# Kernel tuning notes

Measured on AMD Instinct MI355X. Metric: run time of the kernel, lower is better.

The kernel has to match this reference:

```python
import jax, jax.numpy as jnp
import numpy as np

# Config (matches init_kwargs)
B, L, D = 2, 2048, 1024
QH, KVH, HD, FFN = 8, 2, 128, 4096
EPS = 1.1920929e-07  # torch RMSNorm default eps = finfo(float32).eps


def _rope_ts():
    d2 = HD // 2
    freq_exp = (2.0 / HD) * jnp.arange(d2, dtype=jnp.float32)
    return 10000.0 ** freq_exp  # [d2]


def _rope(x):
    # x: [B, L, H, HD], rotated in fp32 (matches x.float() in source)
    d2 = HD // 2
    pos = jnp.arange(L, dtype=jnp.float32)
    rad = pos[:, None] / _rope_ts()[None, :]          # [L, d2]
    s = jnp.sin(rad)[None, :, None, :]                # [1, L, 1, d2]
    c = jnp.cos(rad)[None, :, None, :]
    xf = x.astype(jnp.float32)
    x1, x2 = xf[..., :d2], xf[..., d2:]
    return jnp.concatenate([x1 * c - x2 * s, x2 * c + x1 * s], axis=-1).astype(x.dtype)


def _rmsnorm(x, w):
    xf = x.astype(jnp.float32)
    r = jax.lax.rsqrt(jnp.mean(xf * xf, axis=-1, keepdims=True) + EPS)
    return (xf * r).astype(x.dtype) * w


def setup_inputs() -> dict:
    key = jax.random.key(0)
    ks = jax.random.split(key, 9)
    s = 0.02
    return {
        "x": jax.random.normal(ks[0], (B, L, D), dtype=jnp.float32),
        "ln1_w": jnp.ones((D,), dtype=jnp.float32),
        "wq": jax.random.normal(ks[1], (D, QH * HD), dtype=jnp.float32) * s,
        "wk": jax.random.normal(ks[2], (D, KVH * HD), dtype=jnp.float32) * s,
        "wv": jax.random.normal(ks[3], (D, KVH * HD), dtype=jnp.float32) * s,
        "wo": jax.random.normal(ks[4], (QH * HD, D), dtype=jnp.float32) * s,
        "ln2_w": jnp.ones((D,), dtype=jnp.float32),
        "wg": jax.random.normal(ks[5], (D, FFN), dtype=jnp.float32) * s,
        "wu": jax.random.normal(ks[6], (D, FFN), dtype=jnp.float32) * s,
        "wd": jax.random.normal(ks[7], (FFN, D), dtype=jnp.float32) * s,
    }


def reference(x, ln1_w, wq, wk, wv, wo, ln2_w, wg, wu, wd):
    residual = x
    h = _rmsnorm(x, ln1_w)

    q = _rope((h @ wq).reshape(B, L, QH, HD))          # [B,L,QH,HD]
    k = _rope((h @ wk).reshape(B, L, KVH, HD))         # [B,L,KVH,HD]
    v = (h @ wv).reshape(B, L, KVH, HD)

    rep = QH // KVH  # kv_map = floor(arange(QH)*KVH/QH) == repeat each kv head `rep` times
    qh = jnp.transpose(q, (0, 2, 1, 3)).astype(jnp.float32)                       # [B,QH,L,HD]
    kh = jnp.transpose(jnp.repeat(k, rep, axis=2), (0, 2, 1, 3)).astype(jnp.float32)
    vh = jnp.transpose(jnp.repeat(v, rep, axis=2), (0, 2, 1, 3)).astype(jnp.float32)

    scores = jnp.einsum("bhqd,bhkd->bhqk", qh, kh) / jnp.sqrt(jnp.float32(HD))    # [B,QH,L,L]
    causal = jnp.triu(jnp.ones((L, L), dtype=bool), 1)
    scores = jnp.where(causal, -jnp.inf, scores)
    attn = jax.nn.softmax(scores, axis=-1)
    ctx = jnp.einsum("bhqk,bhkd->bhqd", attn, vh)                                 # [B,QH,L,HD]
    ctx = jnp.transpose(ctx, (0, 2, 1, 3)).reshape(B, L, QH * HD).astype(x.dtype)

    x = ctx @ wo + residual
    residual = x
    h = _rmsnorm(x, ln2_w)
    return (jax.nn.silu(h @ wg) * (h @ wu)) @ wd + residual
```

## Files before the change

kernel.cpp:

```cpp
#include <hip/hip_runtime.h>
#include <hip/hip_bf16.h>
#include <math.h>

#define B_ 2
#define L_ 2048
#define D_ 1024
#define QH_ 8
#define KVH_ 2
#define HD_ 128
#define FFN_ 4096
#define T_ (B_ * L_)
#define EPS_ 1.1920929e-07f

typedef __bf16 bf16x8 __attribute__((ext_vector_type(8)));
typedef float floatx4 __attribute__((ext_vector_type(4)));
typedef unsigned short ushortx8 __attribute__((ext_vector_type(8)));
typedef unsigned short ushortx4 __attribute__((ext_vector_type(4)));

__device__ __forceinline__ unsigned short f2bf(float f) {
  union { float f; unsigned int u; } v;
  v.f = f;
  unsigned int r = v.u + 0x7FFFu + ((v.u >> 16) & 1u);
  return (unsigned short)(r >> 16);
}
__device__ __forceinline__ float bf2f(unsigned short u) {
  union { unsigned int u; float f; } v;
  v.u = ((unsigned int)u) << 16;
  return v.f;
}
__device__ __forceinline__ void gload_lds16(const void* g, void* l) {
  __builtin_amdgcn_global_load_lds((const __attribute__((address_space(1))) void*)g,
                                   (__attribute__((address_space(3))) void*)l, 16, 0, 0);
}

__device__ __forceinline__ void tile_tc(const float* __restrict__ in,
                                        unsigned short* __restrict__ out,
                                        int K, int N, int n0, int k0) {
  __shared__ float tile[32][33];
  int t = threadIdx.x;
  int tx = t & 31, ty = t >> 5;
  for (int r = ty; r < 32; r += 8) tile[r][tx] = in[(size_t)(k0 + r) * N + n0 + tx];
  __syncthreads();
  int nr = t >> 3, kq = t & 7;
  ushortx4 o4;
#pragma unroll
  for (int j = 0; j < 4; j++) o4[j] = f2bf(tile[kq * 4 + j][nr]);
  *(ushortx4*)(out + (size_t)(n0 + nr) * K + k0 + kq * 4) = o4;
}

__device__ __forceinline__ void rmsnorm_row(const float* __restrict__ x,
                                            const float* __restrict__ w,
                                            unsigned short* __restrict__ o, int row) {
  __shared__ float red[4];
  int t = threadIdx.x;
  const float* xr = x + (size_t)row * D_;
  float4 xv = *(const float4*)(xr + t * 4);
  float ss = xv.x * xv.x + xv.y * xv.y + xv.z * xv.z + xv.w * xv.w;
#pragma unroll
  for (int off = 32; off >= 1; off >>= 1) ss += __shfl_xor(ss, off);
  if ((t & 63) == 0) red[t >> 6] = ss;
  __syncthreads();
  float total = red[0] + red[1] + red[2] + red[3];
  float r = rsqrtf(total * (1.0f / (float)D_) + EPS_);
  float4 wv = *(const float4*)(w + t * 4);
  unsigned short* op = o + (size_t)row * D_ + t * 4;
  op[0] = f2bf(xv.x * r * wv.x);
  op[1] = f2bf(xv.y * r * wv.y);
  op[2] = f2bf(xv.z * r * wv.z);
  op[3] = f2bf(xv.w * r * wv.w);
}

__global__ __launch_bounds__(256) void prep_all(
    const float* __restrict__ wq, const float* __restrict__ wk,
    const float* __restrict__ wv, const float* __restrict__ wo,
    const float* __restrict__ wg, const float* __restrict__ wu,
    const float* __restrict__ wd, unsigned short* __restrict__ wT,
    const float* __restrict__ x, const float* __restrict__ ln1w,
    unsigned short* __restrict__ h_bf) {
  int bid = blockIdx.x;
  if (bid < 14848) {
    const float* in;
    unsigned short* out;
    int K, N, nt, base;
    if (bid < 1024)       { in = wq; out = wT;            K = 1024; N = 1024; nt = 32;  base = 0; }
    else if (bid < 1280)  { in = wk; out = wT + 1048576;  K = 1024; N = 256;  nt = 8;   base = 1024; }
    else if (bid < 1536)  { in = wv; out = wT + 1310720;  K = 1024; N = 256;  nt = 8;   base = 1280; }
    else if (bid < 2560)  { in = wo; out = wT + 1572864;  K = 1024; N = 1024; nt = 32;  base = 1536; }
    else if (bid < 6656)  { in = wg; out = wT + 2621440;  K = 1024; N = 4096; nt = 128; base = 2560; }
    else if (bid < 10752) { in = wu; out = wT + 6815744;  K = 1024; N = 4096; nt = 128; base = 6656; }
    else                  { in = wd; out = wT + 11010048; K = 4096; N = 1024; nt = 32;  base = 10752; }
    int idx = bid - base;
    tile_tc(in, out, K, N, (idx % nt) * 32, (idx / nt) * 32);
  } else {
    rmsnorm_row(x, ln1w, h_bf, bid - 14848);
  }
}

__global__ __launch_bounds__(256) void rmsnorm_bf16_kernel(const float* __restrict__ x,
                                                           const float* __restrict__ w,
                                                           unsigned short* __restrict__ o) {
  rmsnorm_row(x, w, o, blockIdx.x);
}

template <int EPI, int MW>
__global__ __launch_bounds__(256) void gemm_bf16(const unsigned short* __restrict__ A,
                                                 const unsigned short* __restrict__ BT,
                                                 const float* __restrict__ R,
                                                 float* __restrict__ C,
                                                 unsigned short* __restrict__ Cb,
                                                 int M, int N, int K) {
  constexpr int AI = MW / 16;
  __shared__ unsigned short As[2][2 * MW * 32];
  __shared__ unsigned short Bs[2][128 * 32];
  int t = threadIdx.x;
  int lane = t & 63, wave = t >> 6;
  int m0 = blockIdx.y * (2 * MW), n0 = blockIdx.x * 128;

  int row_a = t >> 2;
  int kc = ((t & 3) ^ ((t >> 3) & 3)) * 8;
  const unsigned short* ga0 = A + (size_t)(m0 + row_a) * K + kc;
  const unsigned short* ga1 = A + (size_t)(m0 + 64 + row_a) * K + kc;
  const unsigned short* gb0 = BT + (size_t)(n0 + row_a) * K + kc;
  const unsigned short* gb1 = BT + (size_t)(n0 + 64 + row_a) * K + kc;

  int wm = (wave & 1) * MW, wn = (wave >> 1) * 64;
  int fr = lane & 15, quad = lane >> 4;
  int sw = (quad ^ ((fr >> 1) & 3)) * 8;

  floatx4 acc[AI][4];
#pragma unroll
  for (int i = 0; i < AI; i++)
#pragma unroll
    for (int j = 0; j < 4; j++) acc[i][j] = (floatx4){0.f, 0.f, 0.f, 0.f};

  for (int k0 = 0; k0 < K; k0 += 64) {
#pragma unroll
    for (int h = 0; h < 2; h++) {
      int ko = k0 + h * 32;
      gload_lds16(ga0 + ko, As[h] + wave * 512);
      if (MW == 64) gload_lds16(ga1 + ko, As[h] + 2048 + wave * 512);
      gload_lds16(gb0 + ko, Bs[h] + wave * 512);
      gload_lds16(gb1 + ko, Bs[h] + 2048 + wave * 512);
    }
    __syncthreads();
#pragma unroll
    for (int h = 0; h < 2; h++) {
      const unsigned short* arp = As[h] + (size_t)(wm + fr) * 32 + sw;
      const unsigned short* brp = Bs[h] + (size_t)(wn + fr) * 32 + sw;
      bf16x8 af[AI], bfr[4];
#pragma unroll
      for (int i = 0; i < AI; i++)
        af[i] = __builtin_bit_cast(bf16x8, *(const ushortx8*)(arp + i * 16 * 32));
#pragma unroll
      for (int j = 0; j < 4; j++)
        bfr[j] = __builtin_bit_cast(bf16x8, *(const ushortx8*)(brp + j * 16 * 32));
#pragma unroll
      for (int i = 0; i < AI; i++)
#pragma unroll
        for (int j = 0; j < 4; j++)
          acc[i][j] = __builtin_amdgcn_mfma_f32_16x16x32_bf16(af[i], bfr[j], acc[i][j], 0, 0, 0);
    }
    __syncthreads();
  }

  int orow = m0 + wm + quad * 4;
  int ocol = n0 + wn + fr;
#pragma unroll
  for (int i = 0; i < AI; i++) {
#pragma unroll
    for (int r = 0; r < 4; r++) {
      int row = orow + i * 16 + r;
#pragma unroll
      for (int j = 0; j < 4; j++) {
        size_t idx = (size_t)row * N + ocol + j * 16;
        float v = acc[i][j][r];
        if (EPI == 0) C[idx] = v;
        else if (EPI == 1) C[idx] = v + R[idx];
        else if (EPI == 2) C[idx] = v + C[idx];
        else Cb[idx] = f2bf(v);
      }
    }
  }
}

__global__ __launch_bounds__(256, 2) void gemm_gateup(const unsigned short* __restrict__ A,
                                                      const unsigned short* __restrict__ BgT,
                                                      const unsigned short* __restrict__ BuT,
                                                      unsigned short* __restrict__ Cb,
                                                      int M, int K) {
  constexpr int N = FFN_;
  __shared__ unsigned short As[2][128 * 32];
  __shared__ unsigned short Bgs[2][128 * 32];
  __shared__ unsigned short Bus[2][128 * 32];
  int t = threadIdx.x;
  int lane = t & 63, wave = t >> 6;
  int m0 = blockIdx.y * 128, n0 = blockIdx.x * 128;

  int row_a = t >> 2;
  int kc = ((t & 3) ^ ((t >> 3) & 3)) * 8;
  const unsigned short* ga0 = A + (size_t)(m0 + row_a) * K + kc;
  const unsigned short* ga1 = A + (size_t)(m0 + 64 + row_a) * K + kc;
  const unsigned short* gg0 = BgT + (size_t)(n0 + row_a) * K + kc;
  const unsigned short* gg1 = BgT + (size_t)(n0 + 64 + row_a) * K + kc;
  const unsigned short* gu0 = BuT + (size_t)(n0 + row_a) * K + kc;
  const unsigned short* gu1 = BuT + (size_t)(n0 + 64 + row_a) * K + kc;

  int wm = (wave & 1) * 64, wn = (wave >> 1) * 64;
  int fr = lane & 15, quad = lane >> 4;
  int sw = (quad ^ ((fr >> 1) & 3)) * 8;

  floatx4 accg[4][4], accu[4][4];
#pragma unroll
  for (int i = 0; i < 4; i++)
#pragma unroll
    for (int j = 0; j < 4; j++) {
      accg[i][j] = (floatx4){0.f, 0.f, 0.f, 0.f};
      accu[i][j] = (floatx4){0.f, 0.f, 0.f, 0.f};
    }

  for (int k0 = 0; k0 < K; k0 += 64) {
#pragma unroll
    for (int h = 0; h < 2; h++) {
      int ko = k0 + h * 32;
      gload_lds16(ga0 + ko, As[h] + wave * 512);
      gload_lds16(ga1 + ko, As[h] + 2048 + wave * 512);
      gload_lds16(gg0 + ko, Bgs[h] + wave * 512);
      gload_lds16(gg1 + ko, Bgs[h] + 2048 + wave * 512);
      gload_lds16(gu0 + ko, Bus[h] + wave * 512);
      gload_lds16(gu1 + ko, Bus[h] + 2048 + wave * 512);
    }
    __syncthreads();
#pragma unroll
    for (int h = 0; h < 2; h++) {
      const unsigned short* arp = As[h] + (size_t)(wm + fr) * 32 + sw;
      const unsigned short* grp = Bgs[h] + (size_t)(wn + fr) * 32 + sw;
      const unsigned short* urp = Bus[h] + (size_t)(wn + fr) * 32 + sw;
      bf16x8 af[4], bg[4], bu[4];
#pragma unroll
      for (int i = 0; i < 4; i++) {
        af[i] = __builtin_bit_cast(bf16x8, *(const ushortx8*)(arp + i * 16 * 32));
        bg[i] = __builtin_bit_cast(bf16x8, *(const ushortx8*)(grp + i * 16 * 32));
        bu[i] = __builtin_bit_cast(bf16x8, *(const ushortx8*)(urp + i * 16 * 32));
      }
#pragma unroll
      for (int i = 0; i < 4; i++)
#pragma unroll
        for (int j = 0; j < 4; j++) {
          accg[i][j] = __builtin_amdgcn_mfma_f32_16x16x32_bf16(af[i], bg[j], accg[i][j], 0, 0, 0);
          accu[i][j] = __builtin_amdgcn_mfma_f32_16x16x32_bf16(af[i], bu[j], accu[i][j], 0, 0, 0);
        }
    }
    __syncthreads();
  }

  int orow = m0 + wm + quad * 4;
  int ocol = n0 + wn + fr;
#pragma unroll
  for (int i = 0; i < 4; i++) {
#pragma unroll
    for (int r = 0; r < 4; r++) {
      int row = orow + i * 16 + r;
#pragma unroll
      for (int j = 0; j < 4; j++) {
        float g = accg[i][j][r];
        float u = accu[i][j][r];
        Cb[(size_t)row * N + ocol + j * 16] = f2bf(g / (1.f + __expf(-g)) * u);
      }
    }
  }
}

__global__ __launch_bounds__(256) void convert_kv(const unsigned short* __restrict__ qkvb,
                                                  unsigned short* __restrict__ Kb,
                                                  unsigned short* __restrict__ Vt) {
  __shared__ unsigned short tile_s[32][72];
  int bid = blockIdx.x;
  if (bid < 2048) {
    int id = bid * 256 + threadIdx.x;
    int d2 = id & 63;
    int key = (id >> 6) & (L_ - 1);
    int kvh = (id >> 17) & 1;
    int b = id >> 18;
    const unsigned short* src =
        qkvb + (size_t)(b * L_ + key) * 1536 + 1024 + kvh * HD_ + d2;
    float x1 = bf2f(src[0]), x2 = bf2f(src[64]);
    float inv_ts = expf(-0.14391156831f * (float)d2);
    float rad = (float)key * inv_ts;
    float s = sinf(rad), c = cosf(rad);
    unsigned short* dst = Kb + ((size_t)(b * KVH_ + kvh) * L_ + key) * HD_;
    int sw = key & 15;
    dst[((d2 >> 3) ^ sw) * 8 + (d2 & 7)] = f2bf(x1 * c - x2 * s);
    dst[(((d2 >> 3) | 8) ^ sw) * 8 + (d2 & 7)] = f2bf(x2 * c + x1 * s);
  } else {
    int id = bid - 2048;
    int keyt = id & 31, hdt = (id >> 5) & 3, bk = id >> 7;
    int key0 = keyt * 64, hd0 = hdt * 32;
    int b = bk >> 1, kvh = bk & 1;
    int t = threadIdx.x;
    int key_l = t >> 2, hq = t & 3;
    const unsigned short* src = qkvb + (size_t)(b * L_ + key0 + key_l) * 1536 + 1280 +
                                kvh * HD_ + hd0 + hq * 8;
    ushortx8 v8 = *(const ushortx8*)src;
#pragma unroll
    for (int j = 0; j < 8; j++) tile_s[hq * 8 + j][key_l] = v8[j];
    __syncthreads();
    int hdl = t >> 3, cp = t & 7;
    int kc = cp ^ (hdl & 7);
    ushortx8 ob;
#pragma unroll
    for (int j = 0; j < 8; j++) ob[j] = tile_s[hdl][kc * 8 + j];
    *(ushortx8*)(Vt + ((size_t)bk * HD_ + hd0 + hdl) * L_ + key0 + cp * 8) = ob;
  }
}

__global__ __launch_bounds__(256) void attn_mfma(const unsigned short* __restrict__ qkvb,
                                                 const unsigned short* __restrict__ Kb,
                                                 const unsigned short* __restrict__ Vt,
                                                 unsigned short* __restrict__ ctx) {
  __shared__ unsigned short Ks[64 * 128];
  __shared__ unsigned short Vs[128 * 64];
  __shared__ unsigned short Ps[4][16 * 72];
  const float scale = 0.08838834764831843f;
  int id = blockIdx.x;
  int bh = id & 15;
  int p_ = id >> 4;
  int qt = (p_ < 16) ? p_ : 47 - p_;
  int b = bh >> 3, h = bh & 7;
  int bk = b * KVH_ + (h >> 2);
  int q0 = qt * 64;
  int t = threadIdx.x, lane = t & 63, w = t >> 6;
  int fr = lane & 15, quad = lane >> 4;

  int pos = q0 + w * 16 + fr;
  const unsigned short* qrow = qkvb + (size_t)(b * L_ + pos) * 1536 + h * HD_;
  float q32[4][8];
#pragma unroll
  for (int kb = 0; kb < 4; kb++) {
    ushortx8 u = *(const ushortx8*)(qrow + kb * 32 + quad * 8);
#pragma unroll
    for (int j = 0; j < 8; j++) q32[kb][j] = bf2f(u[j]);
  }
  bf16x8 qf[4];
#pragma unroll
  for (int kb2 = 0; kb2 < 2; kb2++) {
#pragma unroll
    for (int j = 0; j < 8; j++) {
      int d2 = kb2 * 32 + quad * 8 + j;
      float inv_ts = expf(-0.14391156831f * (float)d2);
      float rad = (float)pos * inv_ts;
      float s = sinf(rad), c = cosf(rad);
      float x1 = q32[kb2][j], x2 = q32[kb2 + 2][j];
      qf[kb2][j] = (__bf16)((x1 * c - x2 * s) * scale);
      qf[kb2 + 2][j] = (__bf16)((x2 * c + x1 * s) * scale);
    }
  }

  floatx4 o_acc[8];
#pragma unroll
  for (int nt = 0; nt < 8; nt++) o_acc[nt] = (floatx4){0.f, 0.f, 0.f, 0.f};
  float l_r[4] = {0.f, 0.f, 0.f, 0.f};
  unsigned short* Psw = Ps[w];
  const unsigned short* kgb = Kb + (size_t)bk * L_ * HD_;
  const unsigned short* vgb = Vt + (size_t)bk * HD_ * L_;
  int rowg0 = q0 + w * 16 + quad * 4;

  for (int kt = 0; kt <= qt; kt++) {
    int kstart = kt * 64;
    bool diag = (kt == qt);
    __syncthreads();
    const unsigned short* ksrc = kgb + (size_t)kstart * HD_;
#pragma unroll
    for (int it = 0; it < 4; it++) {
      int sl = it * 4 + w;
      gload_lds16(ksrc + sl * 512 + lane * 8, Ks + sl * 512);
    }
#pragma unroll
    for (int it = 0; it < 4; it++) {
      int sl = it * 4 + w;
      gload_lds16(vgb + (size_t)(sl * 8 + (lane >> 3)) * L_ + kstart + (lane & 7) * 8,
                  Vs + sl * 512);
    }
    __syncthreads();

    floatx4 s_acc[4];
#pragma unroll
    for (int jt = 0; jt < 4; jt++) s_acc[jt] = (floatx4){0.f, 0.f, 0.f, 0.f};
#pragma unroll
    for (int kb = 0; kb < 4; kb++) {
#pragma unroll
      for (int jt = 0; jt < 4; jt++) {
        bf16x8 kf = __builtin_bit_cast(
            bf16x8, *(const ushortx8*)(Ks + (jt * 16 + fr) * 128 +
                                       (((kb * 4 + quad) ^ fr) * 8)));
        s_acc[jt] = __builtin_amdgcn_mfma_f32_16x16x32_bf16(qf[kb], kf, s_acc[jt], 0, 0, 0);
      }
    }

#pragma unroll
    for (int jt = 0; jt < 4; jt++) {
#pragma unroll
      for (int r = 0; r < 4; r++) {
        float pp;
        if (diag) {
          int keyg = kstart + jt * 16 + fr;
          pp = (keyg <= rowg0 + r) ? __expf(s_acc[jt][r]) : 0.f;
        } else {
          pp = __expf(s_acc[jt][r]);
        }
        l_r[r] += pp;
        Psw[(quad * 4 + r) * 72 + jt * 16 + fr] = f2bf(pp);
      }
    }
    bf16x8 pf0 = __builtin_bit_cast(bf16x8, *(const ushortx8*)(Psw + fr * 72 + quad * 8));
    bf16x8 pf1 =
        __builtin_bit_cast(bf16x8, *(const ushortx8*)(Psw + fr * 72 + 32 + quad * 8));
#pragma unroll
    for (int nt = 0; nt < 8; nt++) {
      bf16x8 vf0 = __builtin_bit_cast(
          bf16x8,
          *(const ushortx8*)(Vs + (nt * 16 + fr) * 64 + ((quad ^ (fr & 7)) * 8)));
      bf16x8 vf1 = __builtin_bit_cast(
          bf16x8,
          *(const ushortx8*)(Vs + (nt * 16 + fr) * 64 + (((4 + quad) ^ (fr & 7)) * 8)));
      o_acc[nt] = __builtin_amdgcn_mfma_f32_16x16x32_bf16(pf0, vf0, o_acc[nt], 0, 0, 0);
      o_acc[nt] = __builtin_amdgcn_mfma_f32_16x16x32_bf16(pf1, vf1, o_acc[nt], 0, 0, 0);
    }
  }

#pragma unroll
  for (int r = 0; r < 4; r++) {
    l_r[r] += __shfl_xor(l_r[r], 1);
    l_r[r] += __shfl_xor(l_r[r], 2);
    l_r[r] += __shfl_xor(l_r[r], 4);
    l_r[r] += __shfl_xor(l_r[r], 8);
  }

  unsigned short* ob =
      ctx + (size_t)(b * L_ + q0 + w * 16 + quad * 4) * 1024 + h * HD_ + fr;
#pragma unroll
  for (int r = 0; r < 4; r++) {
    float inv = 1.f / l_r[r];
    unsigned short* orow = ob + (size_t)r * 1024;
#pragma unroll
    for (int nt = 0; nt < 8; nt++) orow[nt * 16] = f2bf(o_acc[nt][r] * inv);
  }
}

extern "C" void kernel_launch(void* const* d_in, const int* in_sizes, int n_in,
                              void* d_out, int out_size, void* d_ws, size_t ws_size,
                              hipStream_t stream) {
  const float* x    = (const float*)d_in[0];
  const float* ln1w = (const float*)d_in[1];
  const float* wq   = (const float*)d_in[2];
  const float* wk   = (const float*)d_in[3];
  const float* wvp  = (const float*)d_in[4];
  const float* wo   = (const float*)d_in[5];
  const float* ln2w = (const float*)d_in[6];
  const float* wg   = (const float*)d_in[7];
  const float* wu   = (const float*)d_in[8];
  const float* wd   = (const float*)d_in[9];
  float* out = (float*)d_out;
  char* ws = (char*)d_ws;

  unsigned short* wT = (unsigned short*)ws;
  unsigned short* wqkvT = wT;
  unsigned short* woT = wT + 1572864;
  unsigned short* wgT = wT + 2621440;
  unsigned short* wuT = wT + 6815744;
  unsigned short* wdT = wT + 11010048;
  unsigned short* h_bf = (unsigned short*)(ws + 30408704);
  unsigned short* qkvb = (unsigned short*)(ws + 38797312);
  unsigned short* h2_bf = (unsigned short*)(ws + 51380224);
  unsigned short* Kb = (unsigned short*)(ws + 59768832);
  unsigned short* Vt = (unsigned short*)(ws + 61865984);
  unsigned short* gu = (unsigned short*)(ws + 59768832);
  unsigned short* ctx_bf = h_bf;

  dim3 blk(256);

  prep_all<<<14848 + T_, blk, 0, stream>>>(wq, wk, wvp, wo, wg, wu, wd, wT, x, ln1w, h_bf);
  gemm_bf16<3, 32><<<dim3(12, 64), blk, 0, stream>>>(h_bf, wqkvT, nullptr, nullptr,
                                                     qkvb, T_, 1536, 1024);
  convert_kv<<<2560, blk, 0, stream>>>(qkvb, Kb, Vt);
  attn_mfma<<<512, blk, 0, stream>>>(qkvb, Kb, Vt, ctx_bf);
  gemm_bf16<1, 32><<<dim3(8, 64), blk, 0, stream>>>(ctx_bf, woT, x, out, nullptr,
                                                    T_, 1024, 1024);
  rmsnorm_bf16_kernel<<<T_, blk, 0, stream>>>(out, ln2w, h2_bf);
  gemm_gateup<<<dim3(32, 32), blk, 0, stream>>>(h2_bf, wgT, wuT, gu, T_, 1024);
  gemm_bf16<2, 32><<<dim3(8, 64), blk, 0, stream>>>(gu, wdT, nullptr, out, nullptr,
                                                    T_, 1024, FFN_);
}
```

Measured before the change: 378.3 us.

## Fuse RoPE, scaling and K/V relayout into QKV GEMM epilogue

Adds a dedicated QKV GEMM whose epilogue stages the bf16 tile in LDS, then applies RoPE and the softmax scale to Q and K, writes K in the swizzled layout and V transposed. This removes the separate convert_kv kernel and the RoPE work in the attention prologue, which now just loads pre-rotated Q. It saves one launch and a round trip through the qkv buffer. In exchange the GEMM carries a heavier epilogue, and Q is rounded to bf16 twice (GEMM output, then after rotation).

```diff
diff --git a/kernel.cpp b/kernel.cpp
--- a/kernel.cpp
+++ b/kernel.cpp
@@ -107,7 +107,6 @@
                                                  const unsigned short* __restrict__ BT,
                                                  const float* __restrict__ R,
                                                  float* __restrict__ C,
-                                                 unsigned short* __restrict__ Cb,
                                                  int M, int N, int K) {
   constexpr int AI = MW / 16;
   __shared__ unsigned short As[2][2 * MW * 32];
@@ -174,11 +173,123 @@
       for (int j = 0; j < 4; j++) {
         size_t idx = (size_t)row * N + ocol + j * 16;
         float v = acc[i][j][r];
-        if (EPI == 0) C[idx] = v;
-        else if (EPI == 1) C[idx] = v + R[idx];
-        else if (EPI == 2) C[idx] = v + C[idx];
-        else Cb[idx] = f2bf(v);
+        if (EPI == 1) C[idx] = v + R[idx];
+        else C[idx] = v + C[idx];
       }
+    }
+  }
+}
+
+__global__ __launch_bounds__(256) void gemm_qkv(const unsigned short* __restrict__ A,
+                                                const unsigned short* __restrict__ BT,
+                                                unsigned short* __restrict__ qb,
+                                                unsigned short* __restrict__ Kb,
+                                                unsigned short* __restrict__ Vt) {
+  constexpr int K = 1024;
+  __shared__ unsigned short smem[12288];
+  int t = threadIdx.x;
+  int lane = t & 63, wave = t >> 6;
+  int bx = blockIdx.x;
+  int m0 = blockIdx.y * 64, n0 = bx * 128;
+
+  int row_a = t >> 2;
+  int kc = ((t & 3) ^ ((t >> 3) & 3)) * 8;
+  const unsigned short* ga0 = A + (size_t)(m0 + row_a) * K + kc;
+  const unsigned short* gb0 = BT + (size_t)(n0 + row_a) * K + kc;
+  const unsigned short* gb1 = BT + (size_t)(n0 + 64 + row_a) * K + kc;
+
+  int wm = (wave & 1) * 32, wn = (wave >> 1) * 64;
+  int fr = lane & 15, quad = lane >> 4;
+  int sw = (quad ^ ((fr >> 1) & 3)) * 8;
+
+  floatx4 acc[2][4];
+#pragma unroll
+  for (int i = 0; i < 2; i++)
+#pragma unroll
+    for (int j = 0; j < 4; j++) acc[i][j] = (floatx4){0.f, 0.f, 0.f, 0.f};
+
+  for (int k0 = 0; k0 < K; k0 += 64) {
+#pragma unroll
+    for (int h = 0; h < 2; h++) {
+      int ko = k0 + h * 32;
+      gload_lds16(ga0 + ko, smem + h * 2048 + wave * 512);
+      gload_lds16(gb0 + ko, smem + 4096 + h * 4096 + wave * 512);
+      gload_lds16(gb1 + ko, smem + 4096 + h * 4096 + 2048 + wave * 512);
+    }
+    __syncthreads();
+#pragma unroll
+    for (int h = 0; h < 2; h++) {
+      const unsigned short* arp = smem + h * 2048 + (size_t)(wm + fr) * 32 + sw;
+      const unsigned short* brp = smem + 4096 + h * 4096 + (size_t)(wn + fr) * 32 + sw;
+      bf16x8 af[2], bfr[4];
+#pragma unroll
+      for (int i = 0; i < 2; i++)
+        af[i] = __builtin_bit_cast(bf16x8, *(const ushortx8*)(arp + i * 16 * 32));
+#pragma unroll
+      for (int j = 0; j < 4; j++)
+        bfr[j] = __builtin_bit_cast(bf16x8, *(const ushortx8*)(brp + j * 16 * 32));
+#pragma unroll
+      for (int i = 0; i < 2; i++)
+#pragma unroll
+        for (int j = 0; j < 4; j++)
+          acc[i][j] = __builtin_amdgcn_mfma_f32_16x16x32_bf16(af[i], bfr[j], acc[i][j], 0, 0, 0);
+    }
+    __syncthreads();
+  }
+
+  unsigned short* scr = smem;
+#pragma unroll
+  for (int i = 0; i < 2; i++)
+#pragma unroll
+    for (int r = 0; r < 4; r++)
+#pragma unroll
+      for (int j = 0; j < 4; j++)
+        scr[(size_t)(wm + quad * 4 + i * 16 + r) * 136 + wn + fr + j * 16] =
+            f2bf(acc[i][j][r]);
+  __syncthreads();
+
+  if (bx < 10) {
+    int row = t >> 2, dq = (t & 3) * 16;
+    int tok = m0 + row, pos = tok & (L_ - 1), b = tok >> 11;
+    float scale_ = (bx < 8) ? 0.08838834764831843f : 1.0f;
+    unsigned short lo[16], hi[16];
+#pragma unroll
+    for (int m = 0; m < 16; m++) {
+      int d2 = dq + m;
+      float x1 = bf2f(scr[(size_t)row * 136 + d2]);
+      float x2 = bf2f(scr[(size_t)row * 136 + d2 + 64]);
+      float inv_ts = expf(-0.14391156831f * (float)d2);
+      float rad = (float)pos * inv_ts;
+      float s = sinf(rad), c = cosf(rad);
+      lo[m] = f2bf((x1 * c - x2 * s) * scale_);
+      hi[m] = f2bf((x2 * c + x1 * s) * scale_);
+    }
+    if (bx < 8) {
+      unsigned short* dst = qb + (size_t)tok * 1024 + bx * 128;
+      *(ushortx8*)(dst + dq) = *(const ushortx8*)(lo);
+      *(ushortx8*)(dst + dq + 8) = *(const ushortx8*)(lo + 8);
+      *(ushortx8*)(dst + 64 + dq) = *(const ushortx8*)(hi);
+      *(ushortx8*)(dst + 64 + dq + 8) = *(const ushortx8*)(hi + 8);
+    } else {
+      int kvh = bx - 8, bk = b * KVH_ + kvh, swk = pos & 15;
+      unsigned short* dst = Kb + ((size_t)bk * L_ + pos) * HD_;
+      int c0 = dq >> 3;
+      *(ushortx8*)(dst + ((c0) ^ swk) * 8) = *(const ushortx8*)(lo);
+      *(ushortx8*)(dst + ((c0 + 1) ^ swk) * 8) = *(const ushortx8*)(lo + 8);
+      *(ushortx8*)(dst + ((c0 + 8) ^ swk) * 8) = *(const ushortx8*)(hi);
+      *(ushortx8*)(dst + ((c0 + 9) ^ swk) * 8) = *(const ushortx8*)(hi + 8);
+    }
+  } else {
+    int kvh = bx - 10;
+    int b = m0 >> 11, key0 = m0 & (L_ - 1), bk = b * KVH_ + kvh;
+    int hd = t >> 1, half = t & 1;
+#pragma unroll
+    for (int c = 0; c < 4; c++) {
+      int cp = half * 4 + c, kcc = cp ^ (hd & 7);
+      ushortx8 ob;
+#pragma unroll
+      for (int j = 0; j < 8; j++) ob[j] = scr[(size_t)(kcc * 8 + j) * 136 + hd];
+      *(ushortx8*)(Vt + ((size_t)bk * HD_ + hd) * L_ + key0 + cp * 8) = ob;
     }
   }
 }
@@ -270,57 +381,13 @@
   }
 }
 
-__global__ __launch_bounds__(256) void convert_kv(const unsigned short* __restrict__ qkvb,
-                                                  unsigned short* __restrict__ Kb,
-                                                  unsigned short* __restrict__ Vt) {
-  __shared__ unsigned short tile_s[32][72];
-  int bid = blockIdx.x;
-  if (bid < 2048) {
-    int id = bid * 256 + threadIdx.x;
-    int d2 = id & 63;
-    int key = (id >> 6) & (L_ - 1);
-    int kvh = (id >> 17) & 1;
-    int b = id >> 18;
-    const unsigned short* src =
-        qkvb + (size_t)(b * L_ + key) * 1536 + 1024 + kvh * HD_ + d2;
-    float x1 = bf2f(src[0]), x2 = bf2f(src[64]);
-    float inv_ts = expf(-0.14391156831f * (float)d2);
-    float rad = (float)key * inv_ts;
-    float s = sinf(rad), c = cosf(rad);
-    unsigned short* dst = Kb + ((size_t)(b * KVH_ + kvh) * L_ + key) * HD_;
-    int sw = key & 15;
-    dst[((d2 >> 3) ^ sw) * 8 + (d2 & 7)] = f2bf(x1 * c - x2 * s);
-    dst[(((d2 >> 3) | 8) ^ sw) * 8 + (d2 & 7)] = f2bf(x2 * c + x1 * s);
-  } else {
-    int id = bid - 2048;
-    int keyt = id & 31, hdt = (id >> 5) & 3, bk = id >> 7;
-    int key0 = keyt * 64, hd0 = hdt * 32;
-    int b = bk >> 1, kvh = bk & 1;
-    int t = threadIdx.x;
-    int key_l = t >> 2, hq = t & 3;
-    const unsigned short* src = qkvb + (size_t)(b * L_ + key0 + key_l) * 1536 + 1280 +
-                                kvh * HD_ + hd0 + hq * 8;
-    ushortx8 v8 = *(const ushortx8*)src;
-#pragma unroll
-    for (int j = 0; j < 8; j++) tile_s[hq * 8 + j][key_l] = v8[j];
-    __syncthreads();
-    int hdl = t >> 3, cp = t & 7;
-    int kc = cp ^ (hdl & 7);
-    ushortx8 ob;
-#pragma unroll
-    for (int j = 0; j < 8; j++) ob[j] = tile_s[hdl][kc * 8 + j];
-    *(ushortx8*)(Vt + ((size_t)bk * HD_ + hd0 + hdl) * L_ + key0 + cp * 8) = ob;
-  }
-}
-
-__global__ __launch_bounds__(256) void attn_mfma(const unsigned short* __restrict__ qkvb,
+__global__ __launch_bounds__(256) void attn_mfma(const unsigned short* __restrict__ qb,
                                                  const unsigned short* __restrict__ Kb,
                                                  const unsigned short* __restrict__ Vt,
                                                  unsigned short* __restrict__ ctx) {
   __shared__ unsigned short Ks[64 * 128];
   __shared__ unsigned short Vs[128 * 64];
   __shared__ unsigned short Ps[4][16 * 72];
-  const float scale = 0.08838834764831843f;
   int id = blockIdx.x;
   int bh = id & 15;
   int p_ = id >> 4;
@@ -332,28 +399,11 @@
   int fr = lane & 15, quad = lane >> 4;
 
   int pos = q0 + w * 16 + fr;
-  const unsigned short* qrow = qkvb + (size_t)(b * L_ + pos) * 1536 + h * HD_;
-  float q32[4][8];
-#pragma unroll
-  for (int kb = 0; kb < 4; kb++) {
-    ushortx8 u = *(const ushortx8*)(qrow + kb * 32 + quad * 8);
-#pragma unroll
-    for (int j = 0; j < 8; j++) q32[kb][j] = bf2f(u[j]);
-  }
+  const unsigned short* qrow = qb + (size_t)(b * L_ + pos) * 1024 + h * HD_;
   bf16x8 qf[4];
 #pragma unroll
-  for (int kb2 = 0; kb2 < 2; kb2++) {
-#pragma unroll
-    for (int j = 0; j < 8; j++) {
-      int d2 = kb2 * 32 + quad * 8 + j;
-      float inv_ts = expf(-0.14391156831f * (float)d2);
-      float rad = (float)pos * inv_ts;
-      float s = sinf(rad), c = cosf(rad);
-      float x1 = q32[kb2][j], x2 = q32[kb2 + 2][j];
-      qf[kb2][j] = (__bf16)((x1 * c - x2 * s) * scale);
-      qf[kb2 + 2][j] = (__bf16)((x2 * c + x1 * s) * scale);
-    }
-  }
+  for (int kb = 0; kb < 4; kb++)
+    qf[kb] = __builtin_bit_cast(bf16x8, *(const ushortx8*)(qrow + kb * 32 + quad * 8));
 
   floatx4 o_acc[8];
 #pragma unroll
@@ -469,7 +519,7 @@
   unsigned short* wuT = wT + 6815744;
   unsigned short* wdT = wT + 11010048;
   unsigned short* h_bf = (unsigned short*)(ws + 30408704);
-  unsigned short* qkvb = (unsigned short*)(ws + 38797312);
+  unsigned short* qb = (unsigned short*)(ws + 38797312);
   unsigned short* h2_bf = (unsigned short*)(ws + 51380224);
   unsigned short* Kb = (unsigned short*)(ws + 59768832);
   unsigned short* Vt = (unsigned short*)(ws + 61865984);
@@ -479,14 +529,10 @@
   dim3 blk(256);
 
   prep_all<<<14848 + T_, blk, 0, stream>>>(wq, wk, wvp, wo, wg, wu, wd, wT, x, ln1w, h_bf);
-  gemm_bf16<3, 32><<<dim3(12, 64), blk, 0, stream>>>(h_bf, wqkvT, nullptr, nullptr,
-                                                     qkvb, T_, 1536, 1024);
-  convert_kv<<<2560, blk, 0, stream>>>(qkvb, Kb, Vt);
-  attn_mfma<<<512, blk, 0, stream>>>(qkvb, Kb, Vt, ctx_bf);
-  gemm_bf16<1, 32><<<dim3(8, 64), blk, 0, stream>>>(ctx_bf, woT, x, out, nullptr,
-                                                    T_, 1024, 1024);
+  gemm_qkv<<<dim3(12, 64), blk, 0, stream>>>(h_bf, wqkvT, qb, Kb, Vt);
+  attn_mfma<<<512, blk, 0, stream>>>(qb, Kb, Vt, ctx_bf);
+  gemm_bf16<1, 32><<<dim3(8, 64), blk, 0, stream>>>(ctx_bf, woT, x, out, T_, 1024, 1024);
   rmsnorm_bf16_kernel<<<T_, blk, 0, stream>>>(out, ln2w, h2_bf);
   gemm_gateup<<<dim3(32, 32), blk, 0, stream>>>(h2_bf, wgT, wuT, gu, T_, 1024);
-  gemm_bf16<2, 32><<<dim3(8, 64), blk, 0, stream>>>(gu, wdT, nullptr, out, nullptr,
-                                                    T_, 1024, FFN_);
-}
+  gemm_bf16<2, 32><<<dim3(8, 64), blk, 0, stream>>>(gu, wdT, nullptr, out, T_, 1024, FFN_);
+}
```

New measurement: 373.1 us. No clear change (-1.4%).
